# Optimization experiments

Measured on AMD Instinct MI355X. Metric: run time of the kernel, lower is better.

Reference implementation:

```python
import jax, jax.numpy as jnp
import numpy as np

B, Q, P, HID, H, KV, D = 2, 1024, 3072, 4096, 32, 8, 128
G = H // KV          # GQA group size
EPS = 1e-6
ROPE_THETA = 1e6


def setup_inputs() -> dict:
    key = jax.random.key(0)
    ks = jax.random.split(key, 8)
    hidden_states = jax.random.normal(ks[0], (B, Q, HID), jnp.float32)
    # real RoPE tables for positions [P, P+Q) (extend phase)
    pos = jnp.arange(P, P + Q, dtype=jnp.float32)
    inv_freq = 1.0 / (ROPE_THETA ** (jnp.arange(0, D, 2, dtype=jnp.float32) / D))
    freqs = pos[:, None] * inv_freq[None, :]            # [Q, D/2]
    emb = jnp.concatenate([freqs, freqs], axis=-1)       # [Q, D]
    cos = jnp.broadcast_to(jnp.cos(emb)[None], (B, Q, D)).astype(jnp.float32)
    sin = jnp.broadcast_to(jnp.sin(emb)[None], (B, Q, D)).astype(jnp.float32)
    k_cache = jax.random.normal(ks[1], (B, KV, P, D), jnp.float32)
    v_cache = jax.random.normal(ks[2], (B, KV, P, D), jnp.float32)
    s = 0.02
    Wq = jax.random.normal(ks[3], (HID, H * D), jnp.float32) * s
    Wk = jax.random.normal(ks[4], (HID, KV * D), jnp.float32) * s
    Wv = jax.random.normal(ks[5], (HID, KV * D), jnp.float32) * s
    Wo = jax.random.normal(ks[6], (H * D, HID), jnp.float32) * s
    q_norm_w = jnp.ones((D,), jnp.float32)
    k_norm_w = jnp.ones((D,), jnp.float32)
    return dict(hidden_states=hidden_states, cos=cos, sin=sin,
                k_cache=k_cache, v_cache=v_cache,
                Wq=Wq, Wk=Wk, Wv=Wv, Wo=Wo,
                q_norm_w=q_norm_w, k_norm_w=k_norm_w)


def _rmsnorm(x, w):
    var = jnp.mean(x * x, axis=-1, keepdims=True)
    return x * jax.lax.rsqrt(var + EPS) * w


def _rotate_half(x):
    x1, x2 = jnp.split(x, 2, axis=-1)
    return jnp.concatenate([-x2, x1], axis=-1)


def _rope(x, cos, sin):
    # x: [B, h, Q, D]; cos/sin: [B, Q, D] -> broadcast over heads
    c = cos[:, None, :, :]
    s = sin[:, None, :, :]
    return x * c + _rotate_half(x) * s


def reference(hidden_states, cos, sin, k_cache, v_cache,
              Wq, Wk, Wv, Wo, q_norm_w, k_norm_w):
    # projections
    q = (hidden_states @ Wq).reshape(B, Q, H, D)
    k = (hidden_states @ Wk).reshape(B, Q, KV, D)
    v = (hidden_states @ Wv).reshape(B, Q, KV, D)
    # per-head RMSNorm on q and k
    q = _rmsnorm(q, q_norm_w)
    k = _rmsnorm(k, k_norm_w)
    # [B, heads, Q, D]
    q = q.transpose(0, 2, 1, 3)
    k = k.transpose(0, 2, 1, 3)
    v = v.transpose(0, 2, 1, 3)
    q = _rope(q, cos, sin)
    k = _rope(k, cos, sin)
    # extend: concat cached prefix KV with new KV -> kv_len = P + Q
    K = jnp.concatenate([k_cache, k], axis=2)   # [B, KV, P+Q, D]
    V = jnp.concatenate([v_cache, v], axis=2)
    qg = q.reshape(B, KV, G, Q, D)
    scale = 1.0 / jnp.sqrt(jnp.float32(D))
    scores = jnp.einsum('bkgqd,bksd->bkgqs', qg, K) * scale  # [B,KV,G,Q,P+Q]
    # causal mask offset by prefix: query i sees keys <= P + i
    key_idx = jnp.arange(P + Q)
    mask = key_idx[None, :] <= (P + jnp.arange(Q))[:, None]  # [Q, P+Q]
    scores = jnp.where(mask[None, None, None], scores, jnp.float32(-1e30))
    attn = jax.nn.softmax(scores, axis=-1)
    out = jnp.einsum('bkgqs,bksd->bkgqd', attn, V)           # [B,KV,G,Q,D]
    out = out.reshape(B, H, Q, D).transpose(0, 2, 1, 3).reshape(B, Q, H * D)
    return out @ Wo
```

## Files before the change

### kernel.cpp

```cpp
#include <hip/hip_runtime.h>
#include <hip/hip_bf16.h>

#define B_ 2
#define Q_ 1024
#define P_ 3072
#define HID_ 4096
#define H_ 32
#define KV_ 8
#define D_ 128
#define S_ 4096
#define NQKV 6144
#define QSCALE 0.1275174432f

typedef __attribute__((ext_vector_type(4))) float f32x4;
typedef __attribute__((ext_vector_type(8))) unsigned short u16x8;
typedef __attribute__((ext_vector_type(4))) unsigned short u16x4;
typedef __attribute__((ext_vector_type(8))) __bf16 bf16x8;

__device__ __forceinline__ unsigned short f2bf(float f){
  unsigned u = __builtin_bit_cast(unsigned, f);
  unsigned r = (u + 0x7FFFu + ((u >> 16) & 1u)) >> 16;
  return (unsigned short)r;
}
__device__ __forceinline__ unsigned pk2bf(float lo, float hi){
  unsigned r;
  asm("v_cvt_pk_bf16_f32 %0, %1, %2" : "=v"(r) : "v"(lo), "v"(hi));
  return r;
}
__device__ __forceinline__ f32x4 mfma16(u16x8 a, u16x8 b, f32x4 c){
  return __builtin_amdgcn_mfma_f32_16x16x32_bf16(
      __builtin_bit_cast(bf16x8, a), __builtin_bit_cast(bf16x8, b), c, 0, 0, 0);
}
typedef const __attribute__((address_space(1))) void* gp1_t;
typedef __attribute__((address_space(3))) void* lp3_t;
__device__ __forceinline__ void gl16(const unsigned short* g, unsigned short* l){
  __builtin_amdgcn_global_load_lds((gp1_t)g, (lp3_t)l, 16, 0, 0);
}

__global__ __launch_bounds__(256) void convert_hs(
    const float* __restrict__ X, unsigned short* __restrict__ Hh, int total4){
  for(int i4 = blockIdx.x * 256 + threadIdx.x; i4 < total4; i4 += gridDim.x * 256){
    long i = (long)i4 * 4;
    float4 x = *(const float4*)(X + i);
    *(u16x4*)(Hh + i) = (u16x4){f2bf(x.x), f2bf(x.y), f2bf(x.z), f2bf(x.w)};
  }
}

__global__ __launch_bounds__(256) void convert_wt(
    const float* __restrict__ W, unsigned short* __restrict__ Th, int ldn, int n_off){
  __shared__ float tile[64][65];
  int k0 = blockIdx.y * 64, n0 = blockIdx.x * 64;
  int tid = threadIdx.x;
  int r = tid >> 4, c = (tid & 15) * 4;
  #pragma unroll
  for(int j = 0; j < 4; ++j){
    float4 v = *(const float4*)(W + (long)(k0 + r + j*16) * ldn + n0 + c);
    tile[r + j*16][c] = v.x; tile[r + j*16][c+1] = v.y;
    tile[r + j*16][c+2] = v.z; tile[r + j*16][c+3] = v.w;
  }
  __syncthreads();
  #pragma unroll
  for(int j = 0; j < 4; ++j){
    int n = r + j*16;
    long o = (long)(n_off + n0 + n) * 4096 + k0 + c;
    *(u16x4*)(Th + o) = (u16x4){f2bf(tile[c][n]), f2bf(tile[c+1][n]),
                                f2bf(tile[c+2][n]), f2bf(tile[c+3][n])};
  }
}

__global__ __launch_bounds__(256) void cache_k(
    const float* __restrict__ kc, unsigned short* __restrict__ Kb){
  const int PD = P_ * D_;
  const long SD = (long)S_ * D_;
  int total4 = (B_ * KV_ * PD) >> 2;
  for(int i4 = blockIdx.x * 256 + threadIdx.x; i4 < total4; i4 += gridDim.x * 256){
    long i = (long)i4 * 4;
    int bkv = (int)(i / PD);
    int rem = (int)(i - (long)bkv * PD);
    long dst = (long)bkv * SD + rem;
    float4 k4 = *(const float4*)(kc + i);
    *(u16x4*)(Kb + dst) = (u16x4){f2bf(k4.x), f2bf(k4.y), f2bf(k4.z), f2bf(k4.w)};
  }
}

__global__ __launch_bounds__(256) void cache_vt(
    const float* __restrict__ vc, unsigned short* __restrict__ VT){
  __shared__ unsigned short T[128][72];
  int bkv = blockIdx.y;
  int s0 = blockIdx.x * 64;
  int tid = threadIdx.x;
  int r = tid >> 2, dblk = (tid & 3) * 32;
  const float* src = vc + ((long)bkv * P_ + s0 + r) * 128 + dblk;
  #pragma unroll
  for(int u = 0; u < 8; ++u){
    float4 v = *(const float4*)(src + u*4);
    T[dblk + u*4 + 0][r] = f2bf(v.x);
    T[dblk + u*4 + 1][r] = f2bf(v.y);
    T[dblk + u*4 + 2][r] = f2bf(v.z);
    T[dblk + u*4 + 3][r] = f2bf(v.w);
  }
  __syncthreads();
  int d = tid >> 1, sh = (tid & 1) * 32;
  unsigned short* dst = VT + ((long)bkv * 128 + d) * S_ + s0 + sh;
  #pragma unroll
  for(int u = 0; u < 4; ++u){
    u16x8 v;
    #pragma unroll
    for(int j = 0; j < 8; ++j) v[j] = T[d][sh + u*8 + j];
    *(u16x8*)(dst + u*8) = v;
  }
}

__global__ __launch_bounds__(256) void gemm_bf16(
    const unsigned short* __restrict__ Ag, const unsigned short* __restrict__ Bg,
    float* __restrict__ C, int nbx, int ldc){
  __shared__ __align__(16) unsigned short sA[4096], sB[4096];
  int tid = threadIdx.x;
  int nwg = nbx * 16;
  int lin = blockIdx.x;
  int cpx = nwg >> 3;
  int swz = (lin & 7) * cpx + (lin >> 3);
  int bx = swz % nbx, by = swz / nbx;
  int m0 = by * 128, n0 = bx * 128;
  int lane = tid & 63, w = tid >> 6;
  int lr = lane & 15, lg = lane >> 4;
  int wm = (w >> 1) * 64, wn = (w & 1) * 64;
  int rowi = w * 16 + (lane >> 2);
  int cchunk = ((lane & 3) ^ ((lane >> 3) & 3)) << 3;
  const unsigned short* aP = Ag + (long)(m0 + rowi) * 4096 + cchunk;
  const unsigned short* bP = Bg + (long)(n0 + rowi) * 4096 + cchunk;
  const int step2 = 64 * 4096;
  unsigned short* dA = sA + w * 512;
  unsigned short* dB = sB + w * 512;
  int rdcol = (lg * 8) ^ (((lr >> 1) & 3) << 3);
  f32x4 zero = {0.f,0.f,0.f,0.f};
  f32x4 acc[4][4];
  #pragma unroll
  for(int mi=0;mi<4;++mi)
    #pragma unroll
    for(int ni=0;ni<4;++ni) acc[mi][ni] = zero;

  for(int kt = 0; kt < 128; ++kt){
    int kk = kt * 32;
    __syncthreads();
    gl16(aP + kk, dA);  gl16(aP + step2 + kk, dA + 2048);
    gl16(bP + kk, dB);  gl16(bP + step2 + kk, dB + 2048);
    __syncthreads();
    u16x8 ah[4];
    #pragma unroll
    for(int mi = 0; mi < 4; ++mi)
      ah[mi] = *(const u16x8*)(sA + (wm + mi*16 + lr) * 32 + rdcol);
    #pragma unroll
    for(int ni = 0; ni < 4; ++ni){
      u16x8 bh = *(const u16x8*)(sB + (wn + ni*16 + lr) * 32 + rdcol);
      #pragma unroll
      for(int mi = 0; mi < 4; ++mi)
        acc[mi][ni] = mfma16(ah[mi], bh, acc[mi][ni]);
    }
  }
  #pragma unroll
  for(int mi = 0; mi < 4; ++mi)
    #pragma unroll
    for(int r = 0; r < 4; ++r){
      long rowoff = (long)(m0 + wm + mi*16 + lg*4 + r) * ldc + n0 + wn + lr;
      #pragma unroll
      for(int ni = 0; ni < 4; ++ni)
        C[rowoff + ni*16] = acc[mi][ni][r];
    }
}

__global__ __launch_bounds__(256) void pp_q(
    const float* __restrict__ Craw, const float* __restrict__ cosb,
    const float* __restrict__ sinb, const float* __restrict__ qw,
    unsigned short* __restrict__ Qb){
  int rid = blockIdx.x * 4 + (threadIdx.x >> 6);
  int lane = threadIdx.x & 63;
  int b = rid >> 15;
  int rem = rid & 32767;
  int q = rem >> 5;
  int h = rem & 31;
  long rowoff = (long)(b * Q_ + q) * NQKV + h * 128;
  float x1 = Craw[rowoff + lane];
  float x2 = Craw[rowoff + 64 + lane];
  float ss = x1*x1 + x2*x2;
  for(int o = 32; o; o >>= 1) ss += __shfl_xor(ss, o);
  float norm = rsqrtf(ss * (1.0f/128.0f) + 1e-6f);
  float xn1 = x1 * norm * qw[lane];
  float xn2 = x2 * norm * qw[64 + lane];
  long co = (long)(b * Q_ + q) * 128;
  float c1 = cosb[co + lane],      s1 = sinb[co + lane];
  float c2 = cosb[co + 64 + lane], s2 = sinb[co + 64 + lane];
  float o1 = (xn1 * c1 - xn2 * s1) * QSCALE;
  float o2 = (xn2 * c2 + xn1 * s2) * QSCALE;
  long dst = ((long)(b * H_ + h) * Q_ + q) * 128;
  Qb[dst + lane] = f2bf(o1);
  Qb[dst + 64 + lane] = f2bf(o2);
}

__global__ __launch_bounds__(256) void pp_kv(
    const float* __restrict__ Craw, const float* __restrict__ cosb,
    const float* __restrict__ sinb, const float* __restrict__ kw,
    unsigned short* __restrict__ Kb, unsigned short* __restrict__ VT){
  int rid = blockIdx.x * 4 + (threadIdx.x >> 6);
  int lane = threadIdx.x & 63;
  int b = rid >> 13;
  int rem = rid & 8191;
  int q = rem >> 3;
  int kv = rem & 7;
  int bkv = b * KV_ + kv;
  long rowoff = (long)(b * Q_ + q) * NQKV;
  float x1 = Craw[rowoff + 4096 + kv*128 + lane];
  float x2 = Craw[rowoff + 4096 + kv*128 + 64 + lane];
  float ss = x1*x1 + x2*x2;
  for(int o = 32; o; o >>= 1) ss += __shfl_xor(ss, o);
  float norm = rsqrtf(ss * (1.0f/128.0f) + 1e-6f);
  float xn1 = x1 * norm * kw[lane];
  float xn2 = x2 * norm * kw[64 + lane];
  long co = (long)(b * Q_ + q) * 128;
  float c1 = cosb[co + lane],      s1 = sinb[co + lane];
  float c2 = cosb[co + 64 + lane], s2 = sinb[co + 64 + lane];
  long dst = ((long)bkv * S_ + P_ + q) * 128;
  Kb[dst + lane]      = f2bf(xn1 * c1 - xn2 * s1);
  Kb[dst + 64 + lane] = f2bf(xn2 * c2 + xn1 * s2);
  float v1 = Craw[rowoff + 5120 + kv*128 + lane];
  float v2 = Craw[rowoff + 5120 + kv*128 + 64 + lane];
  VT[((long)bkv * 128 + lane) * S_ + P_ + q]      = f2bf(v1);
  VT[((long)bkv * 128 + 64 + lane) * S_ + P_ + q] = f2bf(v2);
}

#define KVB 32
#define PSL 40
__global__ __launch_bounds__(256) void attn(
    const unsigned short* __restrict__ Qg, const unsigned short* __restrict__ Kg,
    const unsigned short* __restrict__ VTg, unsigned short* __restrict__ Og){
  __shared__ __align__(16) unsigned short Ks[2][KVB*128];
  __shared__ __align__(16) unsigned short Vs[2][128*KVB];
  __shared__ __align__(16) unsigned short Ps[4][32*PSL];
  int tid = threadIdx.x;
  int b = blockIdx.z, h = blockIdx.y, q0 = blockIdx.x * 128;
  int kvh = h >> 2;
  int w = tid >> 6, lane = tid & 63, lr = lane & 15, lg = lane >> 4;
  int q0w = q0 + w * 32;
  u16x8 qh[2][4];
  #pragma unroll
  for(int mi = 0; mi < 2; ++mi){
    long qbase = ((long)(b * H_ + h) * Q_ + q0w + mi*16 + lr) * 128;
    #pragma unroll
    for(int c = 0; c < 4; ++c)
      qh[mi][c] = *(const u16x8*)(Qg + qbase + c*32 + lg*8);
  }
  f32x4 zero = {0.f,0.f,0.f,0.f};
  f32x4 o[2][8];
  #pragma unroll
  for(int mi = 0; mi < 2; ++mi)
    #pragma unroll
    for(int i = 0; i < 8; ++i) o[mi][i] = zero;
  float m[2] = {-3.0e38f, -3.0e38f};
  float l[2] = {0.f, 0.f};
  long kb  = (long)(b * KV_ + kvh) * S_ * 128;
  long vb0 = (long)(b * KV_ + kvh) * 128 * (long)S_;
  int ntiles = 100 + blockIdx.x * 4;
  int koff[2], voff[2], ldst[2];
  #pragma unroll
  for(int i = 0; i < 2; ++i){
    int L = (w*2 + i)*64 + lane;
    ldst[i] = L * 8;
    int r = L >> 4, c8 = (L & 15) ^ (r & 7);
    koff[i] = r*128 + c8*8;
    int d = L >> 2, sc = (L & 3) ^ (d & 3) ^ ((d >> 2) & 3);
    voff[i] = d*S_ + sc*8;
  }
  {
    const unsigned short* kg = Kg + kb;
    const unsigned short* vg = VTg + vb0;
    #pragma unroll
    for(int i = 0; i < 2; ++i){
      gl16(kg + koff[i], &Ks[0][ldst[i]]);
      gl16(vg + voff[i], &Vs[0][ldst[i]]);
    }
  }
  __syncthreads();

  int lr7 = lr & 7;
  for(int t = 0; t < ntiles; ++t){
    int cur = t & 1;
    if(t + 1 < ntiles){
      int s1 = (t + 1) * KVB;
      const unsigned short* kg = Kg + kb + (long)s1 * 128;
      const unsigned short* vg = VTg + vb0 + s1;
      #pragma unroll
      for(int i = 0; i < 2; ++i){
        gl16(kg + koff[i], &Ks[cur^1][ldst[i]]);
        gl16(vg + voff[i], &Vs[cur^1][ldst[i]]);
      }
    }
    int s0 = t * KVB;
    if(s0 <= P_ + q0w + 31){
      f32x4 pacc[2][2];
      pacc[0][0] = zero; pacc[0][1] = zero; pacc[1][0] = zero; pacc[1][1] = zero;
      #pragma unroll
      for(int c = 0; c < 4; ++c)
        #pragma unroll
        for(int ni = 0; ni < 2; ++ni){
          u16x8 kh = *(const u16x8*)(&Ks[cur][(ni*16 + lr)*128 + (((c*4 + lg) ^ lr7) << 3)]);
          pacc[0][ni] = mfma16(kh, qh[0][c], pacc[0][ni]);
          pacc[1][ni] = mfma16(kh, qh[1][c], pacc[1][ni]);
        }
      if(s0 + KVB - 1 > P_ + q0w){
        #pragma unroll
        for(int mi = 0; mi < 2; ++mi){
          int qrow = q0w + mi*16 + lr;
          #pragma unroll
          for(int ni = 0; ni < 2; ++ni)
            #pragma unroll
            for(int r = 0; r < 4; ++r){
              int skey = s0 + ni*16 + lg*4 + r;
              if(skey > P_ + qrow) pacc[mi][ni][r] = -1e30f;
            }
        }
      }
      float tmx[2];
      #pragma unroll
      for(int mi = 0; mi < 2; ++mi){
        float t0 = fmaxf(fmaxf(pacc[mi][0][0], pacc[mi][0][1]),
                         fmaxf(pacc[mi][0][2], pacc[mi][0][3]));
        float t1 = fmaxf(fmaxf(pacc[mi][1][0], pacc[mi][1][1]),
                         fmaxf(pacc[mi][1][2], pacc[mi][1][3]));
        float tm = fmaxf(t0, t1);
        tm = fmaxf(tm, __shfl_xor(tm, 16));
        tm = fmaxf(tm, __shfl_xor(tm, 32));
        tmx[mi] = tm;
      }
      int need = (tmx[0] > m[0] + 8.f) | (tmx[1] > m[1] + 8.f);
      if(__any(need)){
        #pragma unroll
        for(int mi = 0; mi < 2; ++mi){
          float mn = fmaxf(m[mi], tmx[mi]);
          float fac = exp2f(m[mi] - mn);
          m[mi] = mn; l[mi] *= fac;
          #pragma unroll
          for(int r = 0; r < 4; ++r){
            float fr = __shfl(fac, (lg << 4) | (lg*4 + r));
            #pragma unroll
            for(int ni = 0; ni < 8; ++ni) o[mi][ni][r] *= fr;
          }
        }
      }
      #pragma unroll
      for(int mi = 0; mi < 2; ++mi){
        float rs = 0.f;
        #pragma unroll
        for(int ni = 0; ni < 2; ++ni){
          float p0 = exp2f(pacc[mi][ni][0] - m[mi]);
          float p1 = exp2f(pacc[mi][ni][1] - m[mi]);
          float p2 = exp2f(pacc[mi][ni][2] - m[mi]);
          float p3 = exp2f(pacc[mi][ni][3] - m[mi]);
          rs += (p0 + p1) + (p2 + p3);
          uint2 pw; pw.x = pk2bf(p0, p1); pw.y = pk2bf(p2, p3);
          *(uint2*)(&Ps[w][(mi*16 + lr)*PSL + ni*16 + lg*4]) = pw;
        }
        rs += __shfl_xor(rs, 16);
        rs += __shfl_xor(rs, 32);
        l[mi] += rs;
      }
      u16x8 pa0 = *(const u16x8*)(&Ps[w][lr*PSL + lg*8]);
      u16x8 pa1 = *(const u16x8*)(&Ps[w][(16 + lr)*PSL + lg*8]);
      #pragma unroll
      for(int ni = 0; ni < 8; ++ni){
        int d = ni*16 + lr;
        int scs = lg ^ (lr & 3) ^ ((lr >> 2) & 3);
        u16x8 vbf = *(const u16x8*)(&Vs[cur][d*32 + (scs << 3)]);
        o[0][ni] = mfma16(pa0, vbf, o[0][ni]);
        o[1][ni] = mfma16(pa1, vbf, o[1][ni]);
      }
    }
    __syncthreads();
  }
  #pragma unroll
  for(int mi = 0; mi < 2; ++mi){
    float linv = 1.0f / l[mi];
    #pragma unroll
    for(int r = 0; r < 4; ++r){
      float li = __shfl(linv, (lg << 4) | (lg*4 + r));
      int qrow = q0w + mi*16 + lg*4 + r;
      long obase = (long)(b * Q_ + qrow) * 4096 + h * 128;
      #pragma unroll
      for(int ni = 0; ni < 8; ++ni)
        Og[obase + ni*16 + lr] = f2bf(o[mi][ni][r] * li);
    }
  }
}

extern "C" void kernel_launch(void* const* d_in, const int* in_sizes, int n_in,
                              void* d_out, int out_size, void* d_ws, size_t ws_size,
                              hipStream_t stream){
  const float* hs   = (const float*)d_in[0];
  const float* cosb = (const float*)d_in[1];
  const float* sinb = (const float*)d_in[2];
  const float* kc   = (const float*)d_in[3];
  const float* vc   = (const float*)d_in[4];
  const float* Wq   = (const float*)d_in[5];
  const float* Wk   = (const float*)d_in[6];
  const float* Wv   = (const float*)d_in[7];
  const float* Wo   = (const float*)d_in[8];
  const float* qw   = (const float*)d_in[9];
  const float* kw   = (const float*)d_in[10];
  char* ws = (char*)d_ws;
  float* Craw          = (float*)ws;
  unsigned short* OH   = (unsigned short*)ws;
  unsigned short* WTh  = (unsigned short*)(ws + 50331648);
  unsigned short* WoTh = (unsigned short*)(ws + 50331648);
  unsigned short* AH   = (unsigned short*)(ws + 150994944);
  unsigned short* QB   = (unsigned short*)(ws + 150994944);
  unsigned short* KB   = (unsigned short*)(ws + 184549376);
  unsigned short* VT   = (unsigned short*)(ws + 218103808);
  float* Out = (float*)d_out;

  convert_hs<<<dim3(2048), dim3(256), 0, stream>>>(hs, AH, (B_*Q_*HID_)/4);
  convert_wt<<<dim3(64,64), dim3(256), 0, stream>>>(Wq, WTh, 4096, 0);
  convert_wt<<<dim3(16,64), dim3(256), 0, stream>>>(Wk, WTh, 1024, 4096);
  convert_wt<<<dim3(16,64), dim3(256), 0, stream>>>(Wv, WTh, 1024, 5120);
  cache_k<<<dim3(2048), dim3(256), 0, stream>>>(kc, KB);
  cache_vt<<<dim3(48, 16), dim3(256), 0, stream>>>(vc, VT);
  gemm_bf16<<<dim3(768), dim3(256), 0, stream>>>(AH, WTh, Craw, 48, NQKV);
  pp_q<<<dim3(16384), dim3(256), 0, stream>>>(Craw, cosb, sinb, qw, QB);
  pp_kv<<<dim3(4096), dim3(256), 0, stream>>>(Craw, cosb, sinb, kw, KB, VT);
  convert_wt<<<dim3(64,64), dim3(256), 0, stream>>>(Wo, WoTh, 4096, 0);
  attn<<<dim3(8, 32, 2), dim3(256), 0, stream>>>(QB, KB, VT, OH);
  gemm_bf16<<<dim3(512), dim3(256), 0, stream>>>(OH, WoTh, Out, 32, 4096);
}
```

Measured before the change: 564.9 us.

## Split attention KV range across two blocks and use static softmax bound

Attention now splits each query block's KV tiles into two halves handled by separate workgroups, which doubles the grid. Partial outputs and row sums go to fp32 workspace, and a new combine kernel sums them and normalizes. Online-softmax max tracking is replaced by a fixed upper bound on the logits, computed from the max abs of the q/k norm weights, which removes the per-tile max reductions and rescaling. The bound relies on RMS-normalized q and k having a bounded dot product. It adds extra fp32 traffic for the partials plus two small kernel launches.

```diff
diff --git a/kernel.cpp b/kernel.cpp
--- a/kernel.cpp
+++ b/kernel.cpp
@@ -108,6 +108,24 @@
     #pragma unroll
     for(int j = 0; j < 8; ++j) v[j] = T[d][sh + u*8 + j];
     *(u16x8*)(dst + u*8) = v;
+  }
+}
+
+__global__ __launch_bounds__(128) void maxw(
+    const float* __restrict__ qw, const float* __restrict__ kw, float* __restrict__ M){
+  __shared__ float sa[2], sb[2];
+  int t = threadIdx.x;
+  float a = fabsf(qw[t]), b = fabsf(kw[t]);
+  #pragma unroll
+  for(int o = 32; o; o >>= 1){
+    a = fmaxf(a, __shfl_xor(a, o));
+    b = fmaxf(b, __shfl_xor(b, o));
+  }
+  if((t & 63) == 0){ sa[t >> 6] = a; sb[t >> 6] = b; }
+  __syncthreads();
+  if(t == 0){
+    float mq = fmaxf(sa[0], sa[1]), mk = fmaxf(sb[0], sb[1]);
+    M[0] = 128.0f * QSCALE * mq * mk * 1.01f + 0.25f;
   }
 }
 
@@ -232,15 +250,18 @@
 #define PSL 40
 __global__ __launch_bounds__(256) void attn(
     const unsigned short* __restrict__ Qg, const unsigned short* __restrict__ Kg,
-    const unsigned short* __restrict__ VTg, unsigned short* __restrict__ Og){
+    const unsigned short* __restrict__ VTg, const float* __restrict__ Mp,
+    float* __restrict__ po, float* __restrict__ pl){
   __shared__ __align__(16) unsigned short Ks[2][KVB*128];
   __shared__ __align__(16) unsigned short Vs[2][128*KVB];
   __shared__ __align__(16) unsigned short Ps[4][32*PSL];
   int tid = threadIdx.x;
-  int b = blockIdx.z, h = blockIdx.y, q0 = blockIdx.x * 128;
+  int qb = blockIdx.x >> 1, sp = blockIdx.x & 1;
+  int b = blockIdx.z, h = blockIdx.y, q0 = qb * 128;
   int kvh = h >> 2;
   int w = tid >> 6, lane = tid & 63, lr = lane & 15, lg = lane >> 4;
   int q0w = q0 + w * 32;
+  float Mv = Mp[0];
   u16x8 qh[2][4];
   #pragma unroll
   for(int mi = 0; mi < 2; ++mi){
@@ -249,17 +270,20 @@
     for(int c = 0; c < 4; ++c)
       qh[mi][c] = *(const u16x8*)(Qg + qbase + c*32 + lg*8);
   }
+  f32x4 minit = {-Mv, -Mv, -Mv, -Mv};
   f32x4 zero = {0.f,0.f,0.f,0.f};
   f32x4 o[2][8];
   #pragma unroll
   for(int mi = 0; mi < 2; ++mi)
     #pragma unroll
     for(int i = 0; i < 8; ++i) o[mi][i] = zero;
-  float m[2] = {-3.0e38f, -3.0e38f};
   float l[2] = {0.f, 0.f};
   long kb  = (long)(b * KV_ + kvh) * S_ * 128;
   long vb0 = (long)(b * KV_ + kvh) * 128 * (long)S_;
-  int ntiles = 100 + blockIdx.x * 4;
+  int T = 100 + 4 * qb;
+  int half = T >> 1;
+  int t0 = sp ? half : 0;
+  int t1 = sp ? T : half;
   int koff[2], voff[2], ldst[2];
   #pragma unroll
   for(int i = 0; i < 2; ++i){
@@ -271,20 +295,20 @@
     voff[i] = d*S_ + sc*8;
   }
   {
-    const unsigned short* kg = Kg + kb;
-    const unsigned short* vg = VTg + vb0;
+    const unsigned short* kg = Kg + kb + (long)t0 * (KVB*128);
+    const unsigned short* vg = VTg + vb0 + t0 * KVB;
     #pragma unroll
     for(int i = 0; i < 2; ++i){
-      gl16(kg + koff[i], &Ks[0][ldst[i]]);
-      gl16(vg + voff[i], &Vs[0][ldst[i]]);
+      gl16(kg + koff[i], &Ks[t0 & 1][ldst[i]]);
+      gl16(vg + voff[i], &Vs[t0 & 1][ldst[i]]);
     }
   }
   __syncthreads();
 
   int lr7 = lr & 7;
-  for(int t = 0; t < ntiles; ++t){
+  for(int t = t0; t < t1; ++t){
     int cur = t & 1;
-    if(t + 1 < ntiles){
+    if(t + 1 < t1){
       int s1 = (t + 1) * KVB;
       const unsigned short* kg = Kg + kb + (long)s1 * 128;
       const unsigned short* vg = VTg + vb0 + s1;
@@ -297,7 +321,7 @@
     int s0 = t * KVB;
     if(s0 <= P_ + q0w + 31){
       f32x4 pacc[2][2];
-      pacc[0][0] = zero; pacc[0][1] = zero; pacc[1][0] = zero; pacc[1][1] = zero;
+      pacc[0][0] = minit; pacc[0][1] = minit; pacc[1][0] = minit; pacc[1][1] = minit;
       #pragma unroll
       for(int c = 0; c < 4; ++c)
         #pragma unroll
@@ -319,48 +343,19 @@
             }
         }
       }
-      float tmx[2];
-      #pragma unroll
-      for(int mi = 0; mi < 2; ++mi){
-        float t0 = fmaxf(fmaxf(pacc[mi][0][0], pacc[mi][0][1]),
-                         fmaxf(pacc[mi][0][2], pacc[mi][0][3]));
-        float t1 = fmaxf(fmaxf(pacc[mi][1][0], pacc[mi][1][1]),
-                         fmaxf(pacc[mi][1][2], pacc[mi][1][3]));
-        float tm = fmaxf(t0, t1);
-        tm = fmaxf(tm, __shfl_xor(tm, 16));
-        tm = fmaxf(tm, __shfl_xor(tm, 32));
-        tmx[mi] = tm;
-      }
-      int need = (tmx[0] > m[0] + 8.f) | (tmx[1] > m[1] + 8.f);
-      if(__any(need)){
-        #pragma unroll
-        for(int mi = 0; mi < 2; ++mi){
-          float mn = fmaxf(m[mi], tmx[mi]);
-          float fac = exp2f(m[mi] - mn);
-          m[mi] = mn; l[mi] *= fac;
-          #pragma unroll
-          for(int r = 0; r < 4; ++r){
-            float fr = __shfl(fac, (lg << 4) | (lg*4 + r));
-            #pragma unroll
-            for(int ni = 0; ni < 8; ++ni) o[mi][ni][r] *= fr;
-          }
-        }
-      }
       #pragma unroll
       for(int mi = 0; mi < 2; ++mi){
         float rs = 0.f;
         #pragma unroll
         for(int ni = 0; ni < 2; ++ni){
-          float p0 = exp2f(pacc[mi][ni][0] - m[mi]);
-          float p1 = exp2f(pacc[mi][ni][1] - m[mi]);
-          float p2 = exp2f(pacc[mi][ni][2] - m[mi]);
-          float p3 = exp2f(pacc[mi][ni][3] - m[mi]);
+          float p0 = exp2f(pacc[mi][ni][0]);
+          float p1 = exp2f(pacc[mi][ni][1]);
+          float p2 = exp2f(pacc[mi][ni][2]);
+          float p3 = exp2f(pacc[mi][ni][3]);
           rs += (p0 + p1) + (p2 + p3);
           uint2 pw; pw.x = pk2bf(p0, p1); pw.y = pk2bf(p2, p3);
           *(uint2*)(&Ps[w][(mi*16 + lr)*PSL + ni*16 + lg*4]) = pw;
         }
-        rs += __shfl_xor(rs, 16);
-        rs += __shfl_xor(rs, 32);
         l[mi] += rs;
       }
       u16x8 pa0 = *(const u16x8*)(&Ps[w][lr*PSL + lg*8]);
@@ -376,19 +371,40 @@
     }
     __syncthreads();
   }
+  int bh = b * H_ + h;
   #pragma unroll
   for(int mi = 0; mi < 2; ++mi){
-    float linv = 1.0f / l[mi];
+    float lt = l[mi];
+    lt += __shfl_xor(lt, 16);
+    lt += __shfl_xor(lt, 32);
     #pragma unroll
     for(int r = 0; r < 4; ++r){
-      float li = __shfl(linv, (lg << 4) | (lg*4 + r));
       int qrow = q0w + mi*16 + lg*4 + r;
-      long obase = (long)(b * Q_ + qrow) * 4096 + h * 128;
+      long obase = ((long)(sp*64 + bh) * Q_ + qrow) * 128;
       #pragma unroll
       for(int ni = 0; ni < 8; ++ni)
-        Og[obase + ni*16 + lr] = f2bf(o[mi][ni][r] * li);
-    }
-  }
+        po[obase + ni*16 + lr] = o[mi][ni][r];
+    }
+    if(lane < 16)
+      pl[(sp*64 + bh) * Q_ + q0w + mi*16 + lane] = lt;
+  }
+}
+
+__global__ __launch_bounds__(256) void combine(
+    const float* __restrict__ po, const float* __restrict__ pl,
+    unsigned short* __restrict__ OH){
+  int idx = blockIdx.x * 256 + threadIdx.x;
+  int row = idx >> 5;
+  int d4 = (idx & 31) * 4;
+  int bh = row >> 10, q = row & 1023;
+  int b = bh >> 5, h = bh & 31;
+  float lsum = pl[bh*1024 + q] + pl[65536 + bh*1024 + q];
+  float inv = 1.0f / lsum;
+  float4 a = *(const float4*)(po + (long)row*128 + d4);
+  float4 c = *(const float4*)(po + 8388608L + (long)row*128 + d4);
+  u16x4 r = { f2bf((a.x + c.x) * inv), f2bf((a.y + c.y) * inv),
+              f2bf((a.z + c.z) * inv), f2bf((a.w + c.w) * inv) };
+  *(u16x4*)(OH + ((long)(b*1024 + q))*4096 + h*128 + d4) = r;
 }
 
 extern "C" void kernel_launch(void* const* d_in, const int* in_sizes, int n_in,
@@ -408,8 +424,11 @@
   char* ws = (char*)d_ws;
   float* Craw          = (float*)ws;
   unsigned short* OH   = (unsigned short*)ws;
+  float* PL            = (float*)(ws + 16777216);
+  float* MW            = (float*)(ws + 17301504);
   unsigned short* WTh  = (unsigned short*)(ws + 50331648);
   unsigned short* WoTh = (unsigned short*)(ws + 50331648);
+  float* PO            = (float*)(ws + 83886080);
   unsigned short* AH   = (unsigned short*)(ws + 150994944);
   unsigned short* QB   = (unsigned short*)(ws + 150994944);
   unsigned short* KB   = (unsigned short*)(ws + 184549376);
@@ -425,7 +444,9 @@
   gemm_bf16<<<dim3(768), dim3(256), 0, stream>>>(AH, WTh, Craw, 48, NQKV);
   pp_q<<<dim3(16384), dim3(256), 0, stream>>>(Craw, cosb, sinb, qw, QB);
   pp_kv<<<dim3(4096), dim3(256), 0, stream>>>(Craw, cosb, sinb, kw, KB, VT);
+  maxw<<<dim3(1), dim3(128), 0, stream>>>(qw, kw, MW);
   convert_wt<<<dim3(64,64), dim3(256), 0, stream>>>(Wo, WoTh, 4096, 0);
-  attn<<<dim3(8, 32, 2), dim3(256), 0, stream>>>(QB, KB, VT, OH);
+  attn<<<dim3(16, 32, 2), dim3(256), 0, stream>>>(QB, KB, VT, MW, PO, PL);
+  combine<<<dim3(8192), dim3(256), 0, stream>>>(PO, PL, OH);
   gemm_bf16<<<dim3(512), dim3(256), 0, stream>>>(OH, WoTh, Out, 32, 4096);
 }
```

Measured after the change: 537.0 us. 4.9% less time.
